# Performance work log

Measured on AMD Instinct MI355X. Metric: run time of the kernel, lower is better.

Reference implementation:

```python
import jax, jax.numpy as jnp
import numpy as np

SLOPE = 0.01  # LeakyReLU default negative_slope


def _lrelu(x):
    return jnp.where(x >= 0, x, SLOPE * x)


def _similarity(x, w0, w1, w2, w3, w4):
    # stack of bias-free 1x1 convs == channel contractions
    def c(h, w):
        return jnp.einsum('bchw,oc->bohw', h, w)
    h = _lrelu(c(x, w0))
    h = _lrelu(c(h, w1))
    h = _lrelu(c(h, w2))
    h = _lrelu(c(h, w3))
    return c(h, w4)  # [B,1,H,W]


def setup_inputs() -> dict:
    key = jax.random.key(0)
    ks = jax.random.split(key, 7)
    B, C, S = 32, 256, 4

    def kaiming(k, out_c, in_c):
        # kaiming_normal_ mode='fan_out' on a 1x1 conv: std = sqrt(2/out_c)
        return jax.random.normal(k, (out_c, in_c), jnp.float32) * np.sqrt(2.0 / out_c).astype(np.float32)

    return {
        'template_feature': jax.random.normal(ks[0], (B, C, S, S), jnp.float32),
        'candidate_feature': jax.random.normal(ks[1], (B, C, 20, 20), jnp.float32),
        'w0': kaiming(ks[2], 256, 512),
        'w1': kaiming(ks[3], 128, 256),
        'w2': kaiming(ks[4], 64, 128),
        'w3': kaiming(ks[5], 32, 64),
        'w4': kaiming(ks[6], 1, 32),
    }


def reference(template_feature, candidate_feature, w0, w1, w2, w3, w4):
    B, C, S, _ = template_feature.shape  # S == 4
    K = 17  # number of 4x4 patch positions per axis on a 20x20 map

    # ---- template branch ----
    # sum/(H*W) expanded == mean broadcast
    tmean = jnp.mean(template_feature, axis=(2, 3), keepdims=True)
    rep = jnp.concatenate(
        [jnp.broadcast_to(tmean, template_feature.shape), template_feature], axis=1)
    w = _similarity(rep, w0, w1, w2, w3, w4)               # [B,1,S,S]
    wn = jax.nn.softmax(w.reshape(B, -1), axis=1).reshape(B, 1, S, S)
    common_template = jnp.sum(template_feature * wn, axis=(2, 3), keepdims=True)  # [B,C,1,1]
    common_template = jnp.concatenate(
        [common_template, wn.reshape(B, -1, 1, 1)], axis=1)  # [B,C+16,1,1]

    # ---- candidate branch ----
    # torch Unfold(4,4) then view(B,C,4,4,17,17): cfa[b,c,i,j,y,x] = cand[b,c,y+i,x+j]
    patches = jnp.stack(
        [candidate_feature[:, :, i:i + K, j:j + K] for i in range(S) for j in range(S)],
        axis=2)                                             # [B,C,16,K,K]
    cfa = patches.reshape(B, C, S, S, K, K)
    cmean = jnp.mean(cfa, axis=(2, 3), keepdims=True)       # [B,C,1,1,K,K]
    rep_c = jnp.concatenate(
        [jnp.broadcast_to(cmean, cfa.shape), cfa], axis=1)  # [B,2C,S,S,K,K]
    rep_c = rep_c.transpose(0, 4, 5, 1, 2, 3).reshape(B * K * K, 2 * C, S, S)
    wc = _similarity(rep_c, w0, w1, w2, w3, w4)             # [B*K*K,1,S,S]
    wcn = jax.nn.softmax(wc.reshape(B * K * K, -1), axis=1)
    wcn = wcn.reshape(B, K, K, 1, S, S).transpose(0, 3, 4, 5, 1, 2)  # [B,1,S,S,K,K]
    common_candidate = jnp.sum(cfa * wcn, axis=(2, 3), keepdims=True)  # [B,C,1,1,K,K]

    return common_template, common_candidate
```

## Files before the change

### kernel.cpp

```cpp
#include <hip/hip_runtime.h>
#include <hip/hip_bf16.h>
#include <hip/hip_fp16.h>

typedef __attribute__((ext_vector_type(8))) _Float16 half8v;
typedef __attribute__((ext_vector_type(4))) float f32x4;

__device__ __align__(16) float g_w0T[256 * 512];
__device__ __align__(16) unsigned short g_wa0[32 * 8 * 64 * 8];
__device__ __align__(16) unsigned short g_wp1[8 * 8 * 64 * 8];
__device__ __align__(16) unsigned short g_wp2[4 * 4 * 64 * 8];
__device__ __align__(16) unsigned short g_wp3[2 * 2 * 64 * 8];

__device__ __forceinline__ float lrelu(float x) { return x >= 0.f ? x : 0.01f * x; }
__device__ __forceinline__ unsigned short f2hu(float x) {
    _Float16 h = (_Float16)x; return *(unsigned short*)&h;
}
__device__ __forceinline__ unsigned short f2us(float x) {
    __hip_bfloat16 h = __float2bfloat16(x); return *(unsigned short*)&h;
}
__device__ __forceinline__ float us2f(unsigned short u) {
    union { unsigned i; float f; } c; c.i = ((unsigned)u) << 16; return c.f;
}
__device__ __forceinline__ uint2 pack_h4(const f32x4& a) {
    unsigned short h[4];
#pragma unroll
    for (int i = 0; i < 4; ++i) h[i] = f2hu(lrelu(a[i]));
    uint2 r;
    r.x = (unsigned)h[0] | ((unsigned)h[1] << 16);
    r.y = (unsigned)h[2] | ((unsigned)h[3] << 16);
    return r;
}

__global__ __launch_bounds__(256) void prep_kernel(
    const float* __restrict__ w0, const float* __restrict__ w1,
    const float* __restrict__ w2, const float* __restrict__ w3)
{
    int id = blockIdx.x * 256 + threadIdx.x;
    int stride = gridDim.x * 256;
    for (int i = id; i < 256 * 512; i += stride) {
        int c = i >> 9, j = i & 511;
        g_w0T[i] = (j < 256) ? w0[j * 512 + c] : w0[(j - 256) * 512 + 256 + c];
    }
    for (int i = id; i < 32 * 8 * 64 * 8; i += stride) {
        int e = i & 7, l = (i >> 3) & 63, k0 = (i >> 9) & 7, jt = i >> 12;
        int c = k0 * 32 + ((l >> 4) * 8) + e;
        int j = jt * 16 + (l & 15);
        float v = (j < 256) ? w0[j * 512 + c] : w0[(j - 256) * 512 + 256 + c];
        g_wa0[i] = f2hu(v);
    }
    for (int i = id; i < 8 * 8 * 64 * 8; i += stride) {
        int e = i & 7, l = (i >> 3) & 63, k0 = (i >> 9) & 7, m = i >> 12;
        int oc = m * 16 + (l & 15), c = k0 * 32 + ((l >> 4) * 8) + e;
        g_wp1[i] = f2hu(w1[oc * 256 + c]);
    }
    for (int i = id; i < 4 * 4 * 64 * 8; i += stride) {
        int e = i & 7, l = (i >> 3) & 63, k0 = (i >> 9) & 3, m = i >> 11;
        int oc = m * 16 + (l & 15), c = k0 * 32 + ((l >> 4) * 8) + e;
        g_wp2[i] = f2hu(w2[oc * 128 + c]);
    }
    for (int i = id; i < 2 * 2 * 64 * 8; i += stride) {
        int e = i & 7, l = (i >> 3) & 63, k0 = (i >> 9) & 1, m = i >> 10;
        int oc = m * 16 + (l & 15), c = k0 * 32 + ((l >> 4) * 8) + e;
        g_wp3[i] = f2hu(w3[oc * 64 + c]);
    }
}

__global__ __launch_bounds__(256) void a0_kernel(
    const float* __restrict__ cand, float* __restrict__ A0f)
{
    int i = blockIdx.x;
    int idx = (i & 7) * 200 + (i >> 3);
    int b = idx / 50;
    int rest = idx % 50;
    int jh = rest / 25, pq = rest % 25;
    int t = threadIdx.x, l = t & 63, w = t >> 6;
    int col = l & 15, q = l >> 4;
    int pixg = pq * 16 + col;

    const half8v* Ah = (const half8v*)g_wa0;

    f32x4 acc[4];
#pragma unroll
    for (int mt = 0; mt < 4; ++mt) acc[mt] = (f32x4){0.f, 0.f, 0.f, 0.f};

    for (int k0 = 0; k0 < 8; ++k0) {
        const float* cp = cand + ((size_t)(b * 256 + k0 * 32 + q * 8)) * 400 + pixg;
        half8v bv;
#pragma unroll
        for (int e = 0; e < 8; ++e) bv[e] = (_Float16)cp[(size_t)e * 400];
#pragma unroll
        for (int mt = 0; mt < 4; ++mt) {
            int jt = jh * 16 + w * 4 + mt;
            half8v ah = Ah[(jt * 8 + k0) * 64 + l];
            acc[mt] = __builtin_amdgcn_mfma_f32_16x16x32_f16(ah, bv, acc[mt], 0, 0, 0);
        }
    }
    float* dst = A0f + ((size_t)(b * 400) + pixg) * 512 + jh * 256 + w * 64 + q * 4;
#pragma unroll
    for (int mt = 0; mt < 4; ++mt) {
        float4 st = { acc[mt][0], acc[mt][1], acc[mt][2], acc[mt][3] };
        *(float4*)(dst + mt * 16) = st;
    }
}

__global__ __launch_bounds__(256) void transpose_kernel(
    const float* __restrict__ cand, float* __restrict__ ctF,
    unsigned short* __restrict__ ctH, int mode)
{
    __shared__ float tile[64][81];
    int blk = blockIdx.x;
    int b = blk / 20, rest = blk % 20;
    int cg = rest / 5, pg = rest % 5;
    int t = threadIdx.x;
    const float* src = cand + ((size_t)(b * 256 + cg * 64)) * 400 + pg * 80;
#pragma unroll
    for (int k = 0; k < 20; ++k) {
        int idx = k * 256 + t;
        int c = idx / 80, pix = idx % 80;
        tile[c][pix] = src[(size_t)c * 400 + pix];
    }
    __syncthreads();
#pragma unroll
    for (int k = 0; k < 20; ++k) {
        int idx = k * 256 + t;
        int pix = idx >> 6, c = idx & 63;
        float v = tile[c][pix];
        size_t off = ((size_t)(b * 400 + pg * 80 + pix)) * 256 + cg * 64 + c;
        if (mode == 2) ctF[off] = v;
        else           ctH[off] = f2us(v);
    }
}

__global__ __launch_bounds__(512) void persist_kernel(
    const float* __restrict__ cand, const float* __restrict__ w4,
    const float* __restrict__ A0, float* __restrict__ out,
    const float* __restrict__ ctF, const unsigned short* __restrict__ ctH, int mode)
{
    __shared__ __align__(16) char smem[118784];
    const int WA1 = 0, WA2 = 65536, WA3 = 81920, STG = 86016;
    int t = threadIdx.x, l = t & 63, w = t >> 6;

    {
        uint4* d1 = (uint4*)(smem + WA1); const uint4* s1 = (const uint4*)g_wp1;
        for (int i = t; i < 4096; i += 512) d1[i] = s1[i];
        uint4* d2 = (uint4*)(smem + WA2); const uint4* s2 = (const uint4*)g_wp2;
        for (int i = t; i < 1024; i += 512) d2[i] = s2[i];
        uint4* d3 = (uint4*)(smem + WA3); const uint4* s3 = (const uint4*)g_wp3;
        for (int i = t; i < 256; i += 512) d3[i] = s3[i];
    }
    __syncthreads();

    char* bufA = smem + STG + w * 4096;
    char* bufB = bufA + 2048;
    const half8v* A1 = (const half8v*)(smem + WA1);
    const half8v* A2 = (const half8v*)(smem + WA2);
    const half8v* A3 = (const half8v*)(smem + WA3);

    int bid = blockIdx.x;
    int xcd = bid & 7, slot = bid >> 3;
    int p_ = l & 15, q = l >> 4;

    for (int j = slot * 8 + w; j < 1156; j += 256) {
        int idx = xcd * 1156 + j;
        int b = idx / 289, r = idx % 289;
        int y = r / 17, x = r % 17;

        const float* afb = A0 + (size_t)b * 400 * 512;
        int pixo[16];
#pragma unroll
        for (int p = 0; p < 16; ++p) pixo[p] = (y + (p >> 2)) * 20 + x + (p & 3);

        {
            float4 ms = {0.f, 0.f, 0.f, 0.f};
#pragma unroll
            for (int p = 0; p < 16; ++p) {
                float4 v = *(const float4*)(afb + (size_t)pixo[p] * 512 + 4 * l);
                ms.x += v.x; ms.y += v.y; ms.z += v.z; ms.w += v.w;
            }
            ms.x *= 0.0625f; ms.y *= 0.0625f; ms.z *= 0.0625f; ms.w *= 0.0625f;
            *(float4*)(bufB + l * 16) = ms;
        }

        float pxl[16];
#pragma unroll
        for (int p = 0; p < 16; ++p) pxl[p] = afb[(size_t)pixo[p] * 512 + 256 + l];

        f32x4 acc[8];
#pragma unroll
        for (int m = 0; m < 8; ++m) acc[m] = (f32x4){0.f, 0.f, 0.f, 0.f};

#pragma unroll
        for (int qt = 0; qt < 4; ++qt) {
            float m0c = *(const float*)(bufB + (qt * 64 + l) * 4);
#pragma unroll
            for (int p = 0; p < 16; ++p) {
                float h = lrelu(m0c + pxl[p]);
                int off = p * 128 + ((((l >> 3) ^ (p & 7))) << 4) + (l & 7) * 2;
                *(unsigned short*)(bufA + off) = f2hu(h);
            }
            if (qt < 3) {
#pragma unroll
                for (int p = 0; p < 16; ++p)
                    pxl[p] = afb[(size_t)pixo[p] * 512 + 256 + (qt + 1) * 64 + l];
            }
#pragma unroll
            for (int kk = 0; kk < 2; ++kk) {
                int off = p_ * 128 + ((((kk * 4 + q) ^ (p_ & 7))) << 4);
                half8v bq = *(const half8v*)(bufA + off);
                int k0g = qt * 2 + kk;
#pragma unroll
                for (int m = 0; m < 8; ++m) {
                    half8v ah = A1[(m * 8 + k0g) * 64 + l];
                    acc[m] = __builtin_amdgcn_mfma_f32_16x16x32_f16(ah, bq, acc[m], 0, 0, 0);
                }
            }
        }

        f32x4 acc2[4];
#pragma unroll
        for (int m2 = 0; m2 < 4; ++m2) acc2[m2] = (f32x4){0.f, 0.f, 0.f, 0.f};

#pragma unroll
        for (int half = 0; half < 2; ++half) {
#pragma unroll
            for (int mm = 0; mm < 4; ++mm) {
                uint2 ph = pack_h4(acc[half * 4 + mm]);
                int off = p_ * 128 + ((((mm * 2 + (q >> 1)) ^ (p_ & 7))) << 4) + (q & 1) * 8;
                *(uint2*)(bufB + off) = ph;
            }
#pragma unroll
            for (int kf = 0; kf < 2; ++kf) {
                int off = p_ * 128 + ((((kf * 4 + q) ^ (p_ & 7))) << 4);
                half8v bq = *(const half8v*)(bufB + off);
                int kfg = half * 2 + kf;
#pragma unroll
                for (int m2 = 0; m2 < 4; ++m2) {
                    half8v ah = A2[(m2 * 4 + kfg) * 64 + l];
                    acc2[m2] = __builtin_amdgcn_mfma_f32_16x16x32_f16(ah, bq, acc2[m2], 0, 0, 0);
                }
            }
        }

#pragma unroll
        for (int m2 = 0; m2 < 4; ++m2) {
            uint2 ph = pack_h4(acc2[m2]);
            int off = p_ * 128 + ((((m2 * 2 + (q >> 1)) ^ (p_ & 7))) << 4) + (q & 1) * 8;
            *(uint2*)(bufA + off) = ph;
        }
        f32x4 acc3[2];
        acc3[0] = (f32x4){0.f, 0.f, 0.f, 0.f};
        acc3[1] = (f32x4){0.f, 0.f, 0.f, 0.f};
#pragma unroll
        for (int k0 = 0; k0 < 2; ++k0) {
            int off = p_ * 128 + ((((k0 * 4 + q) ^ (p_ & 7))) << 4);
            half8v bq = *(const half8v*)(bufA + off);
#pragma unroll
            for (int mt = 0; mt < 2; ++mt) {
                half8v ah = A3[(mt * 2 + k0) * 64 + l];
                acc3[mt] = __builtin_amdgcn_mfma_f32_16x16x32_f16(ah, bq, acc3[mt], 0, 0, 0);
            }
        }

        float s4 = 0.f;
#pragma unroll
        for (int mt = 0; mt < 2; ++mt)
#pragma unroll
            for (int rg = 0; rg < 4; ++rg)
                s4 += w4[mt * 16 + q * 4 + rg] * lrelu(acc3[mt][rg]);
        s4 += __shfl_xor(s4, 16); s4 += __shfl_xor(s4, 32);
        float mx = s4;
#pragma unroll
        for (int msk = 8; msk; msk >>= 1) mx = fmaxf(mx, __shfl_xor(mx, msk));
        float e = __expf(s4 - mx), sum = e;
#pragma unroll
        for (int msk = 8; msk; msk >>= 1) sum += __shfl_xor(sum, msk);
        float wnl = e / sum;
        if (l < 16) *(float*)(bufB + l * 4) = wnl;
        float wnv[16];
#pragma unroll
        for (int p = 0; p < 16; ++p) wnv[p] = *(const float*)(bufB + p * 4);

        if (mode == 2) {
            const float* ct = ctF + (size_t)b * 400 * 256;
#pragma unroll
            for (int ii = 0; ii < 4; ++ii) {
                float a = 0.f;
#pragma unroll
                for (int p = 0; p < 16; ++p)
                    a += ct[(size_t)pixo[p] * 256 + ii * 64 + l] * wnv[p];
                out[8704 + (size_t)(b * 256 + ii * 64 + l) * 289 + r] = a;
            }
        } else if (mode == 1) {
            const unsigned short* ct = ctH + (size_t)b * 400 * 256;
#pragma unroll
            for (int ii = 0; ii < 4; ++ii) {
                float a = 0.f;
#pragma unroll
                for (int p = 0; p < 16; ++p)
                    a += us2f(ct[(size_t)pixo[p] * 256 + ii * 64 + l]) * wnv[p];
                out[8704 + (size_t)(b * 256 + ii * 64 + l) * 289 + r] = a;
            }
        } else {
            const float* cb = cand + (size_t)b * 256 * 400;
#pragma unroll
            for (int ii = 0; ii < 4; ++ii) {
                int ch = ii * 64 + l;
                const float* cp = cb + (size_t)ch * 400;
                float a = 0.f;
#pragma unroll
                for (int p = 0; p < 16; ++p) a += cp[pixo[p]] * wnv[p];
                out[8704 + (size_t)(b * 256 + ch) * 289 + r] = a;
            }
        }
    }
}

__global__ __launch_bounds__(256) void templ_kernel(
    const float* __restrict__ tf, const float* __restrict__ w4,
    float* __restrict__ out)
{
    __shared__ __align__(16) char smem[17472];
    const int OFF_H0 = 0, OFF_H1 = 8192, OFF_H2 = 12288;
    const int OFF_H3 = 14336, OFF_WN = 16384, OFF_MEAN = 16448;

    int blk = blockIdx.x, t = threadIdx.x;
    int l = t & 63, w = t >> 6;
    int p_ = l & 15, q = l >> 4;
    int b = blk;
    float tpatch[16];

    {
        float* meanp = (float*)(smem + OFF_MEAN);
        float (*patchL)[16] = (float(*)[16])smem;
        const float* src = tf + (size_t)(b * 256 + t) * 16;
        float s = 0.f;
#pragma unroll
        for (int p = 0; p < 16; ++p) {
            float v = src[p];
            tpatch[p] = v; patchL[t][p] = v; s += v;
        }
        meanp[t] = s * (1.f / 16.f);
        __syncthreads();
        float m0 = 0.f, accp[16];
#pragma unroll
        for (int p = 0; p < 16; ++p) accp[p] = 0.f;
        for (int c = 0; c < 256; ++c) {
            float wm = g_w0T[c * 512 + t];
            float wp = g_w0T[c * 512 + 256 + t];
            m0 += wm * meanp[c];
            const float* pr = patchL[c];
#pragma unroll
            for (int p = 0; p < 16; ++p) accp[p] += wp * pr[p];
        }
        __syncthreads();
#pragma unroll
        for (int p = 0; p < 16; ++p) {
            float h = lrelu(m0 + accp[p]);
            int byte = p * 512 + ((((t >> 3) ^ (p & 7))) << 4) + (t & 7) * 2;
            *(unsigned short*)(smem + OFF_H0 + byte) = f2hu(h);
        }
    }
    __syncthreads();

    {
        f32x4 acc0 = {0.f,0.f,0.f,0.f}, acc1 = {0.f,0.f,0.f,0.f};
        const half8v* A1 = (const half8v*)g_wp1;
#pragma unroll
        for (int k0 = 0; k0 < 8; ++k0) {
            int off = p_ * 512 + ((((k0 * 4 + q) ^ (p_ & 7))) << 4);
            half8v bq = *(const half8v*)(smem + OFF_H0 + off);
            half8v ah0 = A1[((2 * w) * 8 + k0) * 64 + l];
            half8v ah1 = A1[((2 * w + 1) * 8 + k0) * 64 + l];
            acc0 = __builtin_amdgcn_mfma_f32_16x16x32_f16(ah0, bq, acc0, 0, 0, 0);
            acc1 = __builtin_amdgcn_mfma_f32_16x16x32_f16(ah1, bq, acc1, 0, 0, 0);
        }
        int gr0 = 2 * (2 * w) + (q >> 1), gr1 = 2 * (2 * w + 1) + (q >> 1);
        uint2 ph0 = pack_h4(acc0), ph1 = pack_h4(acc1);
        int e0 = p_ * 256 + ((gr0 ^ (p_ & 7)) << 4) + (q & 1) * 8;
        int e1 = p_ * 256 + ((gr1 ^ (p_ & 7)) << 4) + (q & 1) * 8;
        *(uint2*)(smem + OFF_H1 + e0) = ph0;
        *(uint2*)(smem + OFF_H1 + e1) = ph1;
    }
    __syncthreads();
    {
        f32x4 acc = {0.f,0.f,0.f,0.f};
        const half8v* A2 = (const half8v*)g_wp2;
#pragma unroll
        for (int k0 = 0; k0 < 4; ++k0) {
            int off = p_ * 256 + ((((k0 * 4 + q) ^ (p_ & 7))) << 4);
            half8v bq = *(const half8v*)(smem + OFF_H1 + off);
            half8v ah = A2[(w * 4 + k0) * 64 + l];
            acc = __builtin_amdgcn_mfma_f32_16x16x32_f16(ah, bq, acc, 0, 0, 0);
        }
        int gr = 2 * w + (q >> 1);
        uint2 ph = pack_h4(acc);
        int e = p_ * 128 + ((gr ^ (p_ & 7)) << 4) + (q & 1) * 8;
        *(uint2*)(smem + OFF_H2 + e) = ph;
    }
    __syncthreads();
    if (w < 2) {
        f32x4 acc = {0.f,0.f,0.f,0.f};
        const half8v* A3 = (const half8v*)g_wp3;
#pragma unroll
        for (int k0 = 0; k0 < 2; ++k0) {
            int off = p_ * 128 + ((((k0 * 4 + q) ^ (p_ & 7))) << 4);
            half8v bq = *(const half8v*)(smem + OFF_H2 + off);
            half8v ah = A3[(w * 2 + k0) * 64 + l];
            acc = __builtin_amdgcn_mfma_f32_16x16x32_f16(ah, bq, acc, 0, 0, 0);
        }
#pragma unroll
        for (int rg = 0; rg < 4; ++rg) {
            float v = lrelu(acc[rg]);
            int oc = w * 16 + q * 4 + rg;
            *(float*)(smem + OFF_H3 + p_ * 128 + ((oc ^ (p_ & 7)) << 2)) = v;
        }
    }
    __syncthreads();
    float* wn = (float*)(smem + OFF_WN);
    if (t < 16) {
        float s4 = 0.f;
#pragma unroll
        for (int c = 0; c < 32; ++c)
            s4 += w4[c] * *(const float*)(smem + OFF_H3 + t * 128 + ((c ^ (t & 7)) << 2));
        float m = s4;
#pragma unroll
        for (int msk = 8; msk; msk >>= 1) m = fmaxf(m, __shfl_xor(m, msk));
        float e = __expf(s4 - m), sum = e;
#pragma unroll
        for (int msk = 8; msk; msk >>= 1) sum += __shfl_xor(sum, msk);
        wn[t] = e / sum;
    }
    __syncthreads();
    float acc = 0.f;
#pragma unroll
    for (int p = 0; p < 16; ++p) acc += tpatch[p] * wn[p];
    out[b * 272 + t] = acc;
    if (t < 16) out[b * 272 + 256 + t] = wn[t];
}

extern "C" void kernel_launch(void* const* d_in, const int* in_sizes, int n_in,
                              void* d_out, int out_size, void* d_ws, size_t ws_size,
                              hipStream_t stream)
{
    const float* tf = (const float*)d_in[0];
    const float* cf = (const float*)d_in[1];
    const float* w0 = (const float*)d_in[2];
    const float* w1 = (const float*)d_in[3];
    const float* w2 = (const float*)d_in[4];
    const float* w3 = (const float*)d_in[5];
    const float* w4 = (const float*)d_in[6];
    float* out = (float*)d_out;
    float* A0f = (float*)d_ws;

    const size_t A0_BYTES = (size_t)32 * 400 * 512 * 4;
    const size_t CT_F32   = (size_t)32 * 400 * 256 * 4;
    const size_t CT_BF16  = (size_t)32 * 400 * 256 * 2;
    int mode = 0;
    if (ws_size >= A0_BYTES + CT_F32)       mode = 2;
    else if (ws_size >= A0_BYTES + CT_BF16) mode = 1;
    float*          ctF = (float*)((char*)d_ws + A0_BYTES);
    unsigned short* ctH = (unsigned short*)((char*)d_ws + A0_BYTES);

    prep_kernel<<<680, 256, 0, stream>>>(w0, w1, w2, w3);
    a0_kernel<<<1600, 256, 0, stream>>>(cf, A0f);
    if (mode) transpose_kernel<<<640, 256, 0, stream>>>(cf, ctF, ctH, mode);
    persist_kernel<<<256, 512, 0, stream>>>(cf, w4, A0f, out, ctF, ctH, mode);
    templ_kernel<<<32, 256, 0, stream>>>(tf, w4, out);
}
```

Baseline: 111.0 us.

## Merge A0, transpose and template kernels; precompute patch means in separate kernel

```diff
diff --git a/kernel.cpp b/kernel.cpp
--- a/kernel.cpp
+++ b/kernel.cpp
@@ -65,76 +65,218 @@
     }
 }
 
-__global__ __launch_bounds__(256) void a0_kernel(
-    const float* __restrict__ cand, float* __restrict__ A0f)
+__global__ __launch_bounds__(256) void front_kernel(
+    const float* __restrict__ cand, const float* __restrict__ tf,
+    const float* __restrict__ w4, float* __restrict__ A0f,
+    float* __restrict__ ctF, unsigned short* __restrict__ ctH, int mode,
+    float* __restrict__ out)
 {
-    int i = blockIdx.x;
-    int idx = (i & 7) * 200 + (i >> 3);
-    int b = idx / 50;
-    int rest = idx % 50;
-    int jh = rest / 25, pq = rest % 25;
-    int t = threadIdx.x, l = t & 63, w = t >> 6;
-    int col = l & 15, q = l >> 4;
-    int pixg = pq * 16 + col;
-
-    const half8v* Ah = (const half8v*)g_wa0;
-
-    f32x4 acc[4];
-#pragma unroll
-    for (int mt = 0; mt < 4; ++mt) acc[mt] = (f32x4){0.f, 0.f, 0.f, 0.f};
-
-    for (int k0 = 0; k0 < 8; ++k0) {
-        const float* cp = cand + ((size_t)(b * 256 + k0 * 32 + q * 8)) * 400 + pixg;
-        half8v bv;
-#pragma unroll
-        for (int e = 0; e < 8; ++e) bv[e] = (_Float16)cp[(size_t)e * 400];
+    __shared__ __align__(16) char fsm[20736];
+    int bid = blockIdx.x;
+    int t = threadIdx.x;
+
+    if (bid < 1600) {
+        int idx = (bid & 7) * 200 + (bid >> 3);
+        int b = idx / 50;
+        int rest = idx % 50;
+        int jh = rest / 25, pq = rest % 25;
+        int l = t & 63, w = t >> 6;
+        int col = l & 15, q = l >> 4;
+        int pixg = pq * 16 + col;
+
+        const half8v* Ah = (const half8v*)g_wa0;
+        f32x4 acc[4];
+#pragma unroll
+        for (int mt = 0; mt < 4; ++mt) acc[mt] = (f32x4){0.f, 0.f, 0.f, 0.f};
+
+        for (int k0 = 0; k0 < 8; ++k0) {
+            const float* cp = cand + ((size_t)(b * 256 + k0 * 32 + q * 8)) * 400 + pixg;
+            half8v bv;
+#pragma unroll
+            for (int e = 0; e < 8; ++e) bv[e] = (_Float16)cp[(size_t)e * 400];
+#pragma unroll
+            for (int mt = 0; mt < 4; ++mt) {
+                int jt = jh * 16 + w * 4 + mt;
+                half8v ah = Ah[(jt * 8 + k0) * 64 + l];
+                acc[mt] = __builtin_amdgcn_mfma_f32_16x16x32_f16(ah, bv, acc[mt], 0, 0, 0);
+            }
+        }
+        float* dst = A0f + ((size_t)(b * 400) + pixg) * 512 + jh * 256 + w * 64 + q * 4;
 #pragma unroll
         for (int mt = 0; mt < 4; ++mt) {
-            int jt = jh * 16 + w * 4 + mt;
-            half8v ah = Ah[(jt * 8 + k0) * 64 + l];
-            acc[mt] = __builtin_amdgcn_mfma_f32_16x16x32_f16(ah, bv, acc[mt], 0, 0, 0);
-        }
-    }
-    float* dst = A0f + ((size_t)(b * 400) + pixg) * 512 + jh * 256 + w * 64 + q * 4;
-#pragma unroll
-    for (int mt = 0; mt < 4; ++mt) {
-        float4 st = { acc[mt][0], acc[mt][1], acc[mt][2], acc[mt][3] };
-        *(float4*)(dst + mt * 16) = st;
-    }
-}
-
-__global__ __launch_bounds__(256) void transpose_kernel(
-    const float* __restrict__ cand, float* __restrict__ ctF,
-    unsigned short* __restrict__ ctH, int mode)
+            float4 st = { acc[mt][0], acc[mt][1], acc[mt][2], acc[mt][3] };
+            *(float4*)(dst + mt * 16) = st;
+        }
+    } else if (bid < 2240) {
+        if (mode == 0) return;
+        float (*tile)[81] = (float(*)[81])fsm;
+        int blk = bid - 1600;
+        int b = blk / 20, rest = blk % 20;
+        int cg = rest / 5, pg = rest % 5;
+        const float* src = cand + ((size_t)(b * 256 + cg * 64)) * 400 + pg * 80;
+#pragma unroll
+        for (int k = 0; k < 20; ++k) {
+            int idx = k * 256 + t;
+            int c = idx / 80, pix = idx % 80;
+            tile[c][pix] = src[(size_t)c * 400 + pix];
+        }
+        __syncthreads();
+#pragma unroll
+        for (int k = 0; k < 20; ++k) {
+            int idx = k * 256 + t;
+            int pix = idx >> 6, c = idx & 63;
+            float v = tile[c][pix];
+            size_t off = ((size_t)(b * 400 + pg * 80 + pix)) * 256 + cg * 64 + c;
+            if (mode == 2) ctF[off] = v;
+            else           ctH[off] = f2us(v);
+        }
+    } else {
+        char* smem = fsm;
+        const int OFF_H0 = 0, OFF_H1 = 8192, OFF_H2 = 12288;
+        const int OFF_H3 = 14336, OFF_WN = 16384, OFF_MEAN = 16448;
+        int l = t & 63, w = t >> 6;
+        int p_ = l & 15, q = l >> 4;
+        int b = bid - 2240;
+        float tpatch[16];
+
+        {
+            float* meanp = (float*)(smem + OFF_MEAN);
+            float (*patchL)[16] = (float(*)[16])smem;
+            const float* src = tf + (size_t)(b * 256 + t) * 16;
+            float s = 0.f;
+#pragma unroll
+            for (int p = 0; p < 16; ++p) {
+                float v = src[p];
+                tpatch[p] = v; patchL[t][p] = v; s += v;
+            }
+            meanp[t] = s * (1.f / 16.f);
+            __syncthreads();
+            float m0 = 0.f, accp[16];
+#pragma unroll
+            for (int p = 0; p < 16; ++p) accp[p] = 0.f;
+            for (int c = 0; c < 256; ++c) {
+                float wm = g_w0T[c * 512 + t];
+                float wp = g_w0T[c * 512 + 256 + t];
+                m0 += wm * meanp[c];
+                const float* pr = patchL[c];
+#pragma unroll
+                for (int p = 0; p < 16; ++p) accp[p] += wp * pr[p];
+            }
+            __syncthreads();
+#pragma unroll
+            for (int p = 0; p < 16; ++p) {
+                float h = lrelu(m0 + accp[p]);
+                int byte = p * 512 + ((((t >> 3) ^ (p & 7))) << 4) + (t & 7) * 2;
+                *(unsigned short*)(smem + OFF_H0 + byte) = f2hu(h);
+            }
+        }
+        __syncthreads();
+
+        {
+            f32x4 acc0 = {0.f,0.f,0.f,0.f}, acc1 = {0.f,0.f,0.f,0.f};
+            const half8v* A1 = (const half8v*)g_wp1;
+#pragma unroll
+            for (int k0 = 0; k0 < 8; ++k0) {
+                int off = p_ * 512 + ((((k0 * 4 + q) ^ (p_ & 7))) << 4);
+                half8v bq = *(const half8v*)(smem + OFF_H0 + off);
+                half8v ah0 = A1[((2 * w) * 8 + k0) * 64 + l];
+                half8v ah1 = A1[((2 * w + 1) * 8 + k0) * 64 + l];
+                acc0 = __builtin_amdgcn_mfma_f32_16x16x32_f16(ah0, bq, acc0, 0, 0, 0);
+                acc1 = __builtin_amdgcn_mfma_f32_16x16x32_f16(ah1, bq, acc1, 0, 0, 0);
+            }
+            int gr0 = 2 * (2 * w) + (q >> 1), gr1 = 2 * (2 * w + 1) + (q >> 1);
+            uint2 ph0 = pack_h4(acc0), ph1 = pack_h4(acc1);
+            int e0 = p_ * 256 + ((gr0 ^ (p_ & 7)) << 4) + (q & 1) * 8;
+            int e1 = p_ * 256 + ((gr1 ^ (p_ & 7)) << 4) + (q & 1) * 8;
+            *(uint2*)(smem + OFF_H1 + e0) = ph0;
+            *(uint2*)(smem + OFF_H1 + e1) = ph1;
+        }
+        __syncthreads();
+        {
+            f32x4 acc = {0.f,0.f,0.f,0.f};
+            const half8v* A2 = (const half8v*)g_wp2;
+#pragma unroll
+            for (int k0 = 0; k0 < 4; ++k0) {
+                int off = p_ * 256 + ((((k0 * 4 + q) ^ (p_ & 7))) << 4);
+                half8v bq = *(const half8v*)(smem + OFF_H1 + off);
+                half8v ah = A2[(w * 4 + k0) * 64 + l];
+                acc = __builtin_amdgcn_mfma_f32_16x16x32_f16(ah, bq, acc, 0, 0, 0);
+            }
+            int gr = 2 * w + (q >> 1);
+            uint2 ph = pack_h4(acc);
+            int e = p_ * 128 + ((gr ^ (p_ & 7)) << 4) + (q & 1) * 8;
+            *(uint2*)(smem + OFF_H2 + e) = ph;
+        }
+        __syncthreads();
+        if (w < 2) {
+            f32x4 acc = {0.f,0.f,0.f,0.f};
+            const half8v* A3 = (const half8v*)g_wp3;
+#pragma unroll
+            for (int k0 = 0; k0 < 2; ++k0) {
+                int off = p_ * 128 + ((((k0 * 4 + q) ^ (p_ & 7))) << 4);
+                half8v bq = *(const half8v*)(smem + OFF_H2 + off);
+                half8v ah = A3[(w * 2 + k0) * 64 + l];
+                acc = __builtin_amdgcn_mfma_f32_16x16x32_f16(ah, bq, acc, 0, 0, 0);
+            }
+#pragma unroll
+            for (int rg = 0; rg < 4; ++rg) {
+                float v = lrelu(acc[rg]);
+                int oc = w * 16 + q * 4 + rg;
+                *(float*)(smem + OFF_H3 + p_ * 128 + ((oc ^ (p_ & 7)) << 2)) = v;
+            }
+        }
+        __syncthreads();
+        float* wn = (float*)(smem + OFF_WN);
+        if (t < 16) {
+            float s4 = 0.f;
+#pragma unroll
+            for (int c = 0; c < 32; ++c)
+                s4 += w4[c] * *(const float*)(smem + OFF_H3 + t * 128 + ((c ^ (t & 7)) << 2));
+            float m = s4;
+#pragma unroll
+            for (int msk = 8; msk; msk >>= 1) m = fmaxf(m, __shfl_xor(m, msk));
+            float e = __expf(s4 - m), sum = e;
+#pragma unroll
+            for (int msk = 8; msk; msk >>= 1) sum += __shfl_xor(sum, msk);
+            wn[t] = e / sum;
+        }
+        __syncthreads();
+        float acc = 0.f;
+#pragma unroll
+        for (int p = 0; p < 16; ++p) acc += tpatch[p] * wn[p];
+        out[b * 272 + t] = acc;
+        if (t < 16) out[b * 272 + 256 + t] = wn[t];
+    }
+}
+
+__global__ __launch_bounds__(256) void m0_kernel(
+    const float* __restrict__ A0f, float* __restrict__ M0)
 {
-    __shared__ float tile[64][81];
-    int blk = blockIdx.x;
-    int b = blk / 20, rest = blk % 20;
-    int cg = rest / 5, pg = rest % 5;
+    int bid = blockIdx.x;
+    int b = bid / 17, y = bid % 17;
     int t = threadIdx.x;
-    const float* src = cand + ((size_t)(b * 256 + cg * 64)) * 400 + pg * 80;
-#pragma unroll
-    for (int k = 0; k < 20; ++k) {
-        int idx = k * 256 + t;
-        int c = idx / 80, pix = idx % 80;
-        tile[c][pix] = src[(size_t)c * 400 + pix];
-    }
-    __syncthreads();
-#pragma unroll
-    for (int k = 0; k < 20; ++k) {
-        int idx = k * 256 + t;
-        int pix = idx >> 6, c = idx & 63;
-        float v = tile[c][pix];
-        size_t off = ((size_t)(b * 400 + pg * 80 + pix)) * 256 + cg * 64 + c;
-        if (mode == 2) ctF[off] = v;
-        else           ctH[off] = f2us(v);
+    const float* base = A0f + (size_t)b * 400 * 512;
+    float cs[20];
+#pragma unroll
+    for (int xx = 0; xx < 20; ++xx) {
+        float s = 0.f;
+#pragma unroll
+        for (int dy = 0; dy < 4; ++dy)
+            s += base[(size_t)((y + dy) * 20 + xx) * 512 + t];
+        cs[xx] = s;
+    }
+#pragma unroll
+    for (int x = 0; x < 17; ++x) {
+        float v = (cs[x] + cs[x + 1] + cs[x + 2] + cs[x + 3]) * 0.0625f;
+        M0[((size_t)(b * 289 + y * 17 + x)) * 256 + t] = v;
     }
 }
 
 __global__ __launch_bounds__(512) void persist_kernel(
     const float* __restrict__ cand, const float* __restrict__ w4,
     const float* __restrict__ A0, float* __restrict__ out,
-    const float* __restrict__ ctF, const unsigned short* __restrict__ ctH, int mode)
+    const float* __restrict__ ctF, const unsigned short* __restrict__ ctH, int mode,
+    const float* __restrict__ M0, int use_m0k)
 {
     __shared__ __align__(16) char smem[118784];
     const int WA1 = 0, WA2 = 65536, WA3 = 81920, STG = 86016;
@@ -170,7 +312,12 @@
 #pragma unroll
         for (int p = 0; p < 16; ++p) pixo[p] = (y + (p >> 2)) * 20 + x + (p & 3);
 
-        {
+        float m0q[4];
+        if (use_m0k) {
+            const float* mp = M0 + (size_t)(b * 289 + r) * 256 + l;
+#pragma unroll
+            for (int qt = 0; qt < 4; ++qt) m0q[qt] = mp[qt * 64];
+        } else {
             float4 ms = {0.f, 0.f, 0.f, 0.f};
 #pragma unroll
             for (int p = 0; p < 16; ++p) {
@@ -191,7 +338,7 @@
 
 #pragma unroll
         for (int qt = 0; qt < 4; ++qt) {
-            float m0c = *(const float*)(bufB + (qt * 64 + l) * 4);
+            float m0c = use_m0k ? m0q[qt] : *(const float*)(bufB + (qt * 64 + l) * 4);
 #pragma unroll
             for (int p = 0; p < 16; ++p) {
                 float h = lrelu(m0c + pxl[p]);
@@ -313,129 +460,6 @@
             }
         }
     }
-}
-
-__global__ __launch_bounds__(256) void templ_kernel(
-    const float* __restrict__ tf, const float* __restrict__ w4,
-    float* __restrict__ out)
-{
-    __shared__ __align__(16) char smem[17472];
-    const int OFF_H0 = 0, OFF_H1 = 8192, OFF_H2 = 12288;
-    const int OFF_H3 = 14336, OFF_WN = 16384, OFF_MEAN = 16448;
-
-    int blk = blockIdx.x, t = threadIdx.x;
-    int l = t & 63, w = t >> 6;
-    int p_ = l & 15, q = l >> 4;
-    int b = blk;
-    float tpatch[16];
-
-    {
-        float* meanp = (float*)(smem + OFF_MEAN);
-        float (*patchL)[16] = (float(*)[16])smem;
-        const float* src = tf + (size_t)(b * 256 + t) * 16;
-        float s = 0.f;
-#pragma unroll
-        for (int p = 0; p < 16; ++p) {
-            float v = src[p];
-            tpatch[p] = v; patchL[t][p] = v; s += v;
-        }
-        meanp[t] = s * (1.f / 16.f);
-        __syncthreads();
-        float m0 = 0.f, accp[16];
-#pragma unroll
-        for (int p = 0; p < 16; ++p) accp[p] = 0.f;
-        for (int c = 0; c < 256; ++c) {
-            float wm = g_w0T[c * 512 + t];
-            float wp = g_w0T[c * 512 + 256 + t];
-            m0 += wm * meanp[c];
-            const float* pr = patchL[c];
-#pragma unroll
-            for (int p = 0; p < 16; ++p) accp[p] += wp * pr[p];
-        }
-        __syncthreads();
-#pragma unroll
-        for (int p = 0; p < 16; ++p) {
-            float h = lrelu(m0 + accp[p]);
-            int byte = p * 512 + ((((t >> 3) ^ (p & 7))) << 4) + (t & 7) * 2;
-            *(unsigned short*)(smem + OFF_H0 + byte) = f2hu(h);
-        }
-    }
-    __syncthreads();
-
-    {
-        f32x4 acc0 = {0.f,0.f,0.f,0.f}, acc1 = {0.f,0.f,0.f,0.f};
-        const half8v* A1 = (const half8v*)g_wp1;
-#pragma unroll
-        for (int k0 = 0; k0 < 8; ++k0) {
-            int off = p_ * 512 + ((((k0 * 4 + q) ^ (p_ & 7))) << 4);
-            half8v bq = *(const half8v*)(smem + OFF_H0 + off);
-            half8v ah0 = A1[((2 * w) * 8 + k0) * 64 + l];
-            half8v ah1 = A1[((2 * w + 1) * 8 + k0) * 64 + l];
-            acc0 = __builtin_amdgcn_mfma_f32_16x16x32_f16(ah0, bq, acc0, 0, 0, 0);
-            acc1 = __builtin_amdgcn_mfma_f32_16x16x32_f16(ah1, bq, acc1, 0, 0, 0);
-        }
-        int gr0 = 2 * (2 * w) + (q >> 1), gr1 = 2 * (2 * w + 1) + (q >> 1);
-        uint2 ph0 = pack_h4(acc0), ph1 = pack_h4(acc1);
-        int e0 = p_ * 256 + ((gr0 ^ (p_ & 7)) << 4) + (q & 1) * 8;
-        int e1 = p_ * 256 + ((gr1 ^ (p_ & 7)) << 4) + (q & 1) * 8;
-        *(uint2*)(smem + OFF_H1 + e0) = ph0;
-        *(uint2*)(smem + OFF_H1 + e1) = ph1;
-    }
-    __syncthreads();
-    {
-        f32x4 acc = {0.f,0.f,0.f,0.f};
-        const half8v* A2 = (const half8v*)g_wp2;
-#pragma unroll
-        for (int k0 = 0; k0 < 4; ++k0) {
-            int off = p_ * 256 + ((((k0 * 4 + q) ^ (p_ & 7))) << 4);
-            half8v bq = *(const half8v*)(smem + OFF_H1 + off);
-            half8v ah = A2[(w * 4 + k0) * 64 + l];
-            acc = __builtin_amdgcn_mfma_f32_16x16x32_f16(ah, bq, acc, 0, 0, 0);
-        }
-        int gr = 2 * w + (q >> 1);
-        uint2 ph = pack_h4(acc);
-        int e = p_ * 128 + ((gr ^ (p_ & 7)) << 4) + (q & 1) * 8;
-        *(uint2*)(smem + OFF_H2 + e) = ph;
-    }
-    __syncthreads();
-    if (w < 2) {
-        f32x4 acc = {0.f,0.f,0.f,0.f};
-        const half8v* A3 = (const half8v*)g_wp3;
-#pragma unroll
-        for (int k0 = 0; k0 < 2; ++k0) {
-            int off = p_ * 128 + ((((k0 * 4 + q) ^ (p_ & 7))) << 4);
-            half8v bq = *(const half8v*)(smem + OFF_H2 + off);
-            half8v ah = A3[(w * 2 + k0) * 64 + l];
-            acc = __builtin_amdgcn_mfma_f32_16x16x32_f16(ah, bq, acc, 0, 0, 0);
-        }
-#pragma unroll
-        for (int rg = 0; rg < 4; ++rg) {
-            float v = lrelu(acc[rg]);
-            int oc = w * 16 + q * 4 + rg;
-            *(float*)(smem + OFF_H3 + p_ * 128 + ((oc ^ (p_ & 7)) << 2)) = v;
-        }
-    }
-    __syncthreads();
-    float* wn = (float*)(smem + OFF_WN);
-    if (t < 16) {
-        float s4 = 0.f;
-#pragma unroll
-        for (int c = 0; c < 32; ++c)
-            s4 += w4[c] * *(const float*)(smem + OFF_H3 + t * 128 + ((c ^ (t & 7)) << 2));
-        float m = s4;
-#pragma unroll
-        for (int msk = 8; msk; msk >>= 1) m = fmaxf(m, __shfl_xor(m, msk));
-        float e = __expf(s4 - m), sum = e;
-#pragma unroll
-        for (int msk = 8; msk; msk >>= 1) sum += __shfl_xor(sum, msk);
-        wn[t] = e / sum;
-    }
-    __syncthreads();
-    float acc = 0.f;
-#pragma unroll
-    for (int p = 0; p < 16; ++p) acc += tpatch[p] * wn[p];
-    out[b * 272 + t] = acc;
-    if (t < 16) out[b * 272 + 256 + t] = wn[t];
 }
 
 extern "C" void kernel_launch(void* const* d_in, const int* in_sizes, int n_in,
@@ -455,15 +479,17 @@
     const size_t A0_BYTES = (size_t)32 * 400 * 512 * 4;
     const size_t CT_F32   = (size_t)32 * 400 * 256 * 4;
     const size_t CT_BF16  = (size_t)32 * 400 * 256 * 2;
-    int mode = 0;
+    const size_t M0_BYTES = (size_t)32 * 289 * 256 * 4;
+    int mode = 0, use_m0k = 0;
     if (ws_size >= A0_BYTES + CT_F32)       mode = 2;
     else if (ws_size >= A0_BYTES + CT_BF16) mode = 1;
+    if (mode == 2 && ws_size >= A0_BYTES + CT_F32 + M0_BYTES) use_m0k = 1;
     float*          ctF = (float*)((char*)d_ws + A0_BYTES);
     unsigned short* ctH = (unsigned short*)((char*)d_ws + A0_BYTES);
+    float*          M0  = (float*)((char*)d_ws + A0_BYTES + CT_F32);
 
     prep_kernel<<<680, 256, 0, stream>>>(w0, w1, w2, w3);
-    a0_kernel<<<1600, 256, 0, stream>>>(cf, A0f);
-    if (mode) transpose_kernel<<<640, 256, 0, stream>>>(cf, ctF, ctH, mode);
-    persist_kernel<<<256, 512, 0, stream>>>(cf, w4, A0f, out, ctF, ctH, mode);
-    templ_kernel<<<32, 256, 0, stream>>>(tf, w4, out);
-}
+    front_kernel<<<2272, 256, 0, stream>>>(cf, tf, w4, A0f, ctF, ctH, mode, out);
+    if (use_m0k) m0_kernel<<<544, 256, 0, stream>>>(A0f, M0);
+    persist_kernel<<<256, 512, 0, stream>>>(cf, w4, A0f, out, ctF, ctH, mode, M0, use_m0k);
+}
```

Result: slower. 115.7 us (+4.3%).
